# Kernel optimization log

Measured on AMD Instinct MI355X. Metric: run time of the kernel, lower is better.

## Reference

```python
import jax, jax.numpy as jnp
import numpy as np

D_MODEL = 512
H = 8


def setup_inputs() -> dict:
    key = jax.random.key(0)
    ks = jax.random.split(key, 11)
    B, L, D = 8, 1024, D_MODEL
    s = 1.0 / np.sqrt(D)
    return {
        "q": jax.random.normal(ks[0], (B, L, D), jnp.float32),
        "k": jax.random.normal(ks[1], (B, L, D), jnp.float32),
        "v": jax.random.normal(ks[2], (B, L, D), jnp.float32),
        "Wq": jax.random.normal(ks[3], (D, D), jnp.float32) * s,
        "bq": jnp.zeros((D,), jnp.float32),
        "Wk": jax.random.normal(ks[4], (D, D), jnp.float32) * s,
        "bk": jnp.zeros((D,), jnp.float32),
        "Wv": jax.random.normal(ks[5], (D, D), jnp.float32) * s,
        "bv": jnp.zeros((D,), jnp.float32),
        "Wo": jax.random.normal(ks[6], (D, D), jnp.float32) * s,
        "bo": jnp.zeros((D,), jnp.float32),
    }


def _split_heads(x, h):
    B, L, D = x.shape
    return x.reshape(B, L, h, D // h).transpose(0, 2, 1, 3)  # (B,h,L,dk)


def reference(q, k, v, Wq, bq, Wk, bk, Wv, bv, Wo, bo):
    B, L, D = q.shape
    dk = D // H
    qw = q @ Wq + bq
    kw = k @ Wk + bk
    vw = q @ Wv + bv  # faithful to source bug: dense_v applied to q, not v
    qh = _split_heads(qw, H)
    kh = _split_heads(kw, H)
    vh = _split_heads(vw, H)
    scale = jnp.asarray(1.0 / np.sqrt(dk), qh.dtype)
    scores = jnp.einsum("bhqd,bhkd->bhqk", qh, kh) * scale  # (B,h,L,L)
    attn = jax.nn.softmax(scores, axis=-1)
    ctx = jnp.einsum("bhqk,bhkd->bhqd", attn, vh)  # (B,h,L,dk)
    out = ctx.transpose(0, 2, 1, 3).reshape(B, L, D) @ Wo + bo
    return out, attn
```

## Files before the change

kernel.cpp:

```cpp
#include <hip/hip_runtime.h>

typedef unsigned short u16;
typedef __bf16 bf16x8 __attribute__((ext_vector_type(8)));
typedef unsigned short u16x8 __attribute__((ext_vector_type(8)));
typedef unsigned short u16x4 __attribute__((ext_vector_type(4)));
typedef float f32x4 __attribute__((ext_vector_type(4)));

#define MFMA16(a, b, c) __builtin_amdgcn_mfma_f32_16x16x32_bf16(a, b, c, 0, 0, 0)

__device__ __forceinline__ u16 f2bf(float f) {
    union { float f; unsigned u; } v; v.f = f;
    unsigned r = v.u + 0x7fffu + ((v.u >> 16) & 1u);
    return (u16)(r >> 16);
}
__device__ __forceinline__ float bf2f(u16 u) {
    union { unsigned u; float f; } v; v.u = (unsigned)u << 16;
    return v.f;
}

typedef __attribute__((address_space(1))) void GAS;
typedef __attribute__((address_space(3))) void LAS;
__device__ __forceinline__ void gload_lds16(const void* g, void* l) {
    __builtin_amdgcn_global_load_lds((GAS*)g, (LAS*)l, 16, 0, 0);
}

__global__ __launch_bounds__(256) void wtrans(const float* Wq, const float* Wk,
                                              const float* Wv, const float* Wo, u16* WT) {
    __shared__ float t[32][33];
    const int z = blockIdx.z;
    const float* W = (z == 0) ? Wq : (z == 1) ? Wk : (z == 2) ? Wv : Wo;
    u16* out = WT + (size_t)z * 512 * 512;
    const int tx = threadIdx.x, ty = threadIdx.y;
    const int k0 = blockIdx.y * 32, n0 = blockIdx.x * 32;
#pragma unroll
    for (int p = 0; p < 4; ++p)
        t[ty + 8 * p][tx] = W[(size_t)(k0 + ty + 8 * p) * 512 + n0 + tx];
    __syncthreads();
#pragma unroll
    for (int p = 0; p < 4; ++p) {
        const int n = n0 + ty + 8 * p;
        out[(size_t)n * 512 + k0 + tx] = f2bf(t[tx][ty + 8 * p]);
    }
}

__global__ __launch_bounds__(256) void qkconv(const float* q, const float* k, u16* qb, u16* kb) {
    const size_t n4 = (size_t)8192 * 512 / 4;
    const size_t stride = (size_t)gridDim.x * 256;
    for (size_t i = (size_t)blockIdx.x * 256 + threadIdx.x; i < 2 * n4; i += stride) {
        const float4 v = (i < n4) ? ((const float4*)q)[i] : ((const float4*)k)[i - n4];
        u16x4 o;
        o[0] = f2bf(v.x); o[1] = f2bf(v.y); o[2] = f2bf(v.z); o[3] = f2bf(v.w);
        if (i < n4) ((u16x4*)qb)[i] = o; else ((u16x4*)kb)[i - n4] = o;
    }
}

__global__ __launch_bounds__(256) void vtrans(const u16* vw, u16* vt) {
    __shared__ u16 t[64][72];
    const int l0 = blockIdx.x * 64, h = blockIdx.y, b = blockIdx.z;
    const int tid = threadIdx.x;
    {
        const int r = tid >> 2, c16 = (tid & 3) * 16;
        const u16* src = vw + (size_t)(b * 1024 + l0 + r) * 512 + h * 64 + c16;
        *(u16x8*)(&t[r][c16])     = *(const u16x8*)(src);
        *(u16x8*)(&t[r][c16 + 8]) = *(const u16x8*)(src + 8);
    }
    __syncthreads();
    {
        const int dk = tid >> 2, lc = (tid & 3) * 16;
        u16x8 a0, a1;
#pragma unroll
        for (int e = 0; e < 8; ++e) { a0[e] = t[lc + e][dk]; a1[e] = t[lc + 8 + e][dk]; }
        u16* dst = vt + ((size_t)(b * 8 + h) * 64 + dk) * 1024 + l0 + lc;
        *(u16x8*)dst       = a0;
        *(u16x8*)(dst + 8) = a1;
    }
}

template <bool C_F32>
__device__ __forceinline__ void gemm_core(const u16* A, const u16* Bt,
                                          const float* bias, void* Cp,
                                          int bm, int bn) {
    __shared__ u16 As[128 * 64];
    __shared__ u16 Bs[128 * 64];
    const int tid  = threadIdx.x;
    const int lane = tid & 63;
    const int w    = tid >> 6;
    const int wm   = (w >> 1) * 64;
    const int wn   = (w & 1) * 64;
    const int col  = lane & 15;
    const int quad = lane >> 4;
    const int srow = lane >> 3;
    const int scol = (lane & 7) * 8;

    f32x4 acc[4][4] = {};

    for (int kt = 0; kt < 512; kt += 64) {
        __syncthreads();
#pragma unroll
        for (int p = 0; p < 4; ++p) {
            const int c  = w * 4 + p;
            const int gr = c * 8 + srow;
            gload_lds16(A  + (size_t)(bm * 128 + gr) * 512 + kt + scol, As + c * 512);
            gload_lds16(Bt + (size_t)(bn * 128 + gr) * 512 + kt + scol, Bs + c * 512);
        }
        __syncthreads();
#pragma unroll
        for (int ks = 0; ks < 2; ++ks) {
            const int k0 = ks * 32 + quad * 8;
            bf16x8 af[4], bfr[4];
#pragma unroll
            for (int i = 0; i < 4; ++i)
                af[i] = __builtin_bit_cast(bf16x8, *(const u16x8*)(As + (wm + i * 16 + col) * 64 + k0));
#pragma unroll
            for (int j = 0; j < 4; ++j)
                bfr[j] = __builtin_bit_cast(bf16x8, *(const u16x8*)(Bs + (wn + j * 16 + col) * 64 + k0));
#pragma unroll
            for (int i = 0; i < 4; ++i)
#pragma unroll
                for (int j = 0; j < 4; ++j)
                    acc[i][j] = MFMA16(af[i], bfr[j], acc[i][j]);
        }
    }
#pragma unroll
    for (int j = 0; j < 4; ++j) {
        const int gn = bn * 128 + wn + j * 16 + col;
        const float bv = bias[gn];
#pragma unroll
        for (int i = 0; i < 4; ++i) {
#pragma unroll
            for (int r = 0; r < 4; ++r) {
                const int gm = bm * 128 + wm + i * 16 + quad * 4 + r;
                const float val = acc[i][j][r] + bv;
                if (C_F32) ((float*)Cp)[(size_t)gm * 512 + gn] = val;
                else       ((u16*)Cp)[(size_t)gm * 512 + gn]   = f2bf(val);
            }
        }
    }
}

__global__ __launch_bounds__(256, 3) void qkv_gemm(const u16* qb, const u16* kb, const u16* WT,
                                                   const float* bq, const float* bk, const float* bv,
                                                   u16* out) {
    const int z = blockIdx.z;
    const u16* A      = (z == 1) ? kb : qb;
    const u16* B      = WT + (size_t)z * 512 * 512;
    const float* bias = (z == 0) ? bq : (z == 1) ? bk : bv;
    u16* C            = out + (size_t)z * 8192 * 512;
    gemm_core<false>(A, B, bias, C, blockIdx.x, blockIdx.y);
}

__global__ __launch_bounds__(256, 3) void out_gemm(const u16* ctx, const u16* WoT,
                                                   const float* bo, float* out) {
    gemm_core<true>(ctx, WoT, bo, out, blockIdx.x, blockIdx.y);
}

__global__ __launch_bounds__(512, 4) void attn_kernel(const u16* qw, const u16* kw, const u16* vt,
                                                      float* attn_out, u16* ctx) {
    __shared__ u16 Ks[128 * 72];
    __shared__ u16 Vs[64 * 136];
    __shared__ u16 Ps[8][16 * 136];

    const int qt  = blockIdx.x;
    const int bh  = blockIdx.y;
    const int b   = bh >> 3, h = bh & 7;
    const int tid = threadIdx.x;
    const int lane = tid & 63, w = tid >> 6;
    const int col = lane & 15, quad = lane >> 4;
    const int wq  = w * 16;
    const float scale = 0.125f;

    const size_t headbase = (size_t)b * (1024 * 512) + (size_t)h * 64;
    const u16* vh = vt + (size_t)bh * (64 * 1024);

    const int krow = tid >> 2, koff = (tid & 3) * 16;
    const int vrow = tid >> 3, voff = (tid & 7) * 16;
    const u16* kbase = kw + headbase + (size_t)krow * 512 + koff;
    const u16* vbase = vh + (size_t)vrow * 1024 + voff;

    bf16x8 qf[2];
    {
        const u16* qp = qw + headbase + (size_t)(qt * 128 + wq + col) * 512 + quad * 8;
        qf[0] = __builtin_bit_cast(bf16x8, *(const u16x8*)qp);
        qf[1] = __builtin_bit_cast(bf16x8, *(const u16x8*)(qp + 32));
    }

    float l_acc[4] = {0.f, 0.f, 0.f, 0.f};

    u16x8 rk0 = *(const u16x8*)kbase;
    u16x8 rk1 = *(const u16x8*)(kbase + 8);
    for (int kt = 0; kt < 8; ++kt) {
        __syncthreads();
        *(u16x8*)(Ks + krow * 72 + koff)     = rk0;
        *(u16x8*)(Ks + krow * 72 + koff + 8) = rk1;
        __syncthreads();
        if (kt < 7) {
            const u16* kp = kbase + (size_t)(kt + 1) * (128 * 512);
            rk0 = *(const u16x8*)kp;
            rk1 = *(const u16x8*)(kp + 8);
        }
        f32x4 s[8] = {};
#pragma unroll
        for (int ks = 0; ks < 2; ++ks) {
            const int k0 = ks * 32 + quad * 8;
#pragma unroll
            for (int j = 0; j < 8; ++j) {
                const bf16x8 kf = __builtin_bit_cast(bf16x8,
                    *(const u16x8*)(Ks + (j * 16 + col) * 72 + k0));
                s[j] = MFMA16(qf[ks], kf, s[j]);
            }
        }
#pragma unroll
        for (int j = 0; j < 8; ++j)
#pragma unroll
            for (int r = 0; r < 4; ++r)
                l_acc[r] += __expf(s[j][r] * scale);
    }

    float rinv[4];
#pragma unroll
    for (int r = 0; r < 4; ++r) {
        float l = l_acc[r];
        l += __shfl_xor(l, 1); l += __shfl_xor(l, 2);
        l += __shfl_xor(l, 4); l += __shfl_xor(l, 8);
        rinv[r] = 1.0f / l;
    }

    f32x4 o[4] = {};

    rk0 = *(const u16x8*)kbase;
    rk1 = *(const u16x8*)(kbase + 8);
    u16x8 rv0 = *(const u16x8*)vbase;
    u16x8 rv1 = *(const u16x8*)(vbase + 8);
    for (int kt = 0; kt < 8; ++kt) {
        __syncthreads();
        *(u16x8*)(Ks + krow * 72 + koff)      = rk0;
        *(u16x8*)(Ks + krow * 72 + koff + 8)  = rk1;
        *(u16x8*)(Vs + vrow * 136 + voff)     = rv0;
        *(u16x8*)(Vs + vrow * 136 + voff + 8) = rv1;
        __syncthreads();
        if (kt < 7) {
            const u16* kp = kbase + (size_t)(kt + 1) * (128 * 512);
            rk0 = *(const u16x8*)kp;
            rk1 = *(const u16x8*)(kp + 8);
            const u16* vp = vbase + (kt + 1) * 128;
            rv0 = *(const u16x8*)vp;
            rv1 = *(const u16x8*)(vp + 8);
        }
        u16* pw = &Ps[w][0];
#pragma unroll
        for (int half = 0; half < 2; ++half) {
            f32x4 s[4] = {};
#pragma unroll
            for (int ks = 0; ks < 2; ++ks) {
                const int k0 = ks * 32 + quad * 8;
#pragma unroll
                for (int j = 0; j < 4; ++j) {
                    const bf16x8 kf = __builtin_bit_cast(bf16x8,
                        *(const u16x8*)(Ks + (half * 64 + j * 16 + col) * 72 + k0));
                    s[j] = MFMA16(qf[ks], kf, s[j]);
                }
            }
#pragma unroll
            for (int j = 0; j < 4; ++j)
#pragma unroll
                for (int r = 0; r < 4; ++r) {
                    const float p = __expf(s[j][r] * scale) * rinv[r];
                    pw[(quad * 4 + r) * 136 + half * 64 + j * 16 + col] = f2bf(p);
                }
        }
        {
            const int rl = lane >> 2, c0 = (lane & 3) * 4;
            float* ao = attn_out + ((size_t)bh * 1024 + (size_t)(qt * 128 + wq + rl)) * 1024
                        + (size_t)kt * 128 + c0;
#pragma unroll
            for (int it = 0; it < 8; ++it) {
                const u16x4 pv = *(const u16x4*)(pw + rl * 136 + it * 16 + c0);
                float4 f;
                f.x = bf2f(pv[0]); f.y = bf2f(pv[1]); f.z = bf2f(pv[2]); f.w = bf2f(pv[3]);
                *(float4*)(ao + it * 16) = f;
            }
        }
#pragma unroll
        for (int ks = 0; ks < 4; ++ks) {
            const int k0 = ks * 32 + quad * 8;
            const bf16x8 pf = __builtin_bit_cast(bf16x8, *(const u16x8*)(pw + col * 136 + k0));
#pragma unroll
            for (int j = 0; j < 4; ++j) {
                const bf16x8 vf = __builtin_bit_cast(bf16x8,
                    *(const u16x8*)(Vs + (j * 16 + col) * 136 + k0));
                o[j] = MFMA16(pf, vf, o[j]);
            }
        }
    }

#pragma unroll
    for (int j = 0; j < 4; ++j)
#pragma unroll
        for (int r = 0; r < 4; ++r) {
            const int qg = qt * 128 + wq + quad * 4 + r;
            ctx[(size_t)(b * 1024 + qg) * 512 + h * 64 + j * 16 + col] = f2bf(o[j][r]);
        }
}

extern "C" void kernel_launch(void* const* d_in, const int* in_sizes, int n_in,
                              void* d_out, int out_size, void* d_ws, size_t ws_size,
                              hipStream_t stream) {
    (void)in_sizes; (void)n_in; (void)out_size; (void)ws_size;
    const float* q  = (const float*)d_in[0];
    const float* k  = (const float*)d_in[1];
    const float* Wq = (const float*)d_in[3];
    const float* bq = (const float*)d_in[4];
    const float* Wk = (const float*)d_in[5];
    const float* bk = (const float*)d_in[6];
    const float* Wv = (const float*)d_in[7];
    const float* bv = (const float*)d_in[8];
    const float* Wo = (const float*)d_in[9];
    const float* bo = (const float*)d_in[10];

    float* out  = (float*)d_out;
    float* attn = (float*)d_out + (size_t)8 * 1024 * 512;

    char* ws = (char*)d_ws;
    u16* WT  = (u16*)ws;
    u16* qb  = (u16*)(ws + (size_t)2 * 1024 * 1024);
    u16* kb  = qb + (size_t)8192 * 512;
    u16* qkv = kb + (size_t)8192 * 512;
    u16* qw  = qkv;
    u16* kw  = qkv + (size_t)8192 * 512;
    u16* vw  = qkv + (size_t)2 * 8192 * 512;
    u16* ctx = qkv + (size_t)3 * 8192 * 512;
    u16* vt  = qkv + (size_t)4 * 8192 * 512;

    wtrans     <<<dim3(16, 16, 4), dim3(32, 8), 0, stream>>>(Wq, Wk, Wv, Wo, WT);
    qkconv     <<<dim3(2048),      256,          0, stream>>>(q, k, qb, kb);
    qkv_gemm   <<<dim3(64, 4, 3),  256,          0, stream>>>(qb, kb, WT, bq, bk, bv, qkv);
    vtrans     <<<dim3(16, 8, 8),  256,          0, stream>>>(vw, vt);
    attn_kernel<<<dim3(8, 64),     512,          0, stream>>>(qw, kw, vt, attn, ctx);
    out_gemm   <<<dim3(64, 4),     256,          0, stream>>>(ctx, WT + (size_t)3 * 512 * 512, bo, out);
}
```

Baseline: 415.7 us.

## Transpose score MFMA layout, vectorize P stores, nontemporal attn writes, swap grid order

Swaps the MFMA operands so each lane holds four consecutive key columns of one query row. The row-sum reduction then needs fewer shuffles, and P can be written to LDS as packed 4-element vectors instead of scattered scalar stores. The attention-matrix write-out now has each half-wave cover a full 128-column row segment, which gives contiguous 512-byte stores, and uses nontemporal stores to avoid polluting the cache. The launch grid is reordered so consecutive blocks span different heads, and bf16 rounding moves to the hardware conversion builtin.

```diff
diff --git a/kernel.cpp b/kernel.cpp
--- a/kernel.cpp
+++ b/kernel.cpp
@@ -16,6 +16,9 @@
 __device__ __forceinline__ float bf2f(u16 u) {
     union { unsigned u; float f; } v; v.u = (unsigned)u << 16;
     return v.f;
+}
+__device__ __forceinline__ u16 bfc(float f) {
+    return __builtin_bit_cast(u16, (__bf16)f);
 }
 
 typedef __attribute__((address_space(1))) void GAS;
@@ -160,8 +163,8 @@
     __shared__ u16 Vs[64 * 136];
     __shared__ u16 Ps[8][16 * 136];
 
-    const int qt  = blockIdx.x;
-    const int bh  = blockIdx.y;
+    const int bh  = blockIdx.x;
+    const int qt  = blockIdx.y;
     const int b   = bh >> 3, h = bh & 7;
     const int tid = threadIdx.x;
     const int lane = tid & 63, w = tid >> 6;
@@ -184,7 +187,7 @@
         qf[1] = __builtin_bit_cast(bf16x8, *(const u16x8*)(qp + 32));
     }
 
-    float l_acc[4] = {0.f, 0.f, 0.f, 0.f};
+    float l_acc = 0.f;
 
     u16x8 rk0 = *(const u16x8*)kbase;
     u16x8 rk1 = *(const u16x8*)(kbase + 8);
@@ -206,23 +209,21 @@
             for (int j = 0; j < 8; ++j) {
                 const bf16x8 kf = __builtin_bit_cast(bf16x8,
                     *(const u16x8*)(Ks + (j * 16 + col) * 72 + k0));
-                s[j] = MFMA16(qf[ks], kf, s[j]);
+                s[j] = MFMA16(kf, qf[ks], s[j]);
             }
         }
 #pragma unroll
         for (int j = 0; j < 8; ++j)
 #pragma unroll
             for (int r = 0; r < 4; ++r)
-                l_acc[r] += __expf(s[j][r] * scale);
-    }
-
-    float rinv[4];
-#pragma unroll
-    for (int r = 0; r < 4; ++r) {
-        float l = l_acc[r];
-        l += __shfl_xor(l, 1); l += __shfl_xor(l, 2);
-        l += __shfl_xor(l, 4); l += __shfl_xor(l, 8);
-        rinv[r] = 1.0f / l;
+                l_acc += __expf(s[j][r] * scale);
+    }
+
+    float rinv;
+    {
+        float l = l_acc;
+        l += __shfl_xor(l, 16); l += __shfl_xor(l, 32);
+        rinv = 1.0f / l;
     }
 
     f32x4 o[4] = {};
@@ -257,27 +258,31 @@
                 for (int j = 0; j < 4; ++j) {
                     const bf16x8 kf = __builtin_bit_cast(bf16x8,
                         *(const u16x8*)(Ks + (half * 64 + j * 16 + col) * 72 + k0));
-                    s[j] = MFMA16(qf[ks], kf, s[j]);
+                    s[j] = MFMA16(kf, qf[ks], s[j]);
                 }
             }
 #pragma unroll
-            for (int j = 0; j < 4; ++j)
-#pragma unroll
-                for (int r = 0; r < 4; ++r) {
-                    const float p = __expf(s[j][r] * scale) * rinv[r];
-                    pw[(quad * 4 + r) * 136 + half * 64 + j * 16 + col] = f2bf(p);
-                }
+            for (int j = 0; j < 4; ++j) {
+                u16x4 pk;
+                pk[0] = bfc(__expf(s[j][0] * scale) * rinv);
+                pk[1] = bfc(__expf(s[j][1] * scale) * rinv);
+                pk[2] = bfc(__expf(s[j][2] * scale) * rinv);
+                pk[3] = bfc(__expf(s[j][3] * scale) * rinv);
+                *(u16x4*)(pw + col * 136 + half * 64 + j * 16 + quad * 4) = pk;
+            }
         }
         {
-            const int rl = lane >> 2, c0 = (lane & 3) * 4;
-            float* ao = attn_out + ((size_t)bh * 1024 + (size_t)(qt * 128 + wq + rl)) * 1024
-                        + (size_t)kt * 128 + c0;
+            const int r2 = lane >> 5;
+            const int c0 = (lane & 31) * 4;
+            float* ao = attn_out + ((size_t)bh * 1024 + (size_t)(qt * 128 + wq)) * 1024
+                        + (size_t)kt * 128;
 #pragma unroll
             for (int it = 0; it < 8; ++it) {
-                const u16x4 pv = *(const u16x4*)(pw + rl * 136 + it * 16 + c0);
-                float4 f;
-                f.x = bf2f(pv[0]); f.y = bf2f(pv[1]); f.z = bf2f(pv[2]); f.w = bf2f(pv[3]);
-                *(float4*)(ao + it * 16) = f;
+                const int row = it * 2 + r2;
+                const u16x4 pv = *(const u16x4*)(pw + row * 136 + c0);
+                f32x4 f;
+                f[0] = bf2f(pv[0]); f[1] = bf2f(pv[1]); f[2] = bf2f(pv[2]); f[3] = bf2f(pv[3]);
+                __builtin_nontemporal_store(f, (f32x4*)(ao + (size_t)row * 1024 + c0));
             }
         }
 #pragma unroll
@@ -335,6 +340,6 @@
     qkconv     <<<dim3(2048),      256,          0, stream>>>(q, k, qb, kb);
     qkv_gemm   <<<dim3(64, 4, 3),  256,          0, stream>>>(qb, kb, WT, bq, bk, bv, qkv);
     vtrans     <<<dim3(16, 8, 8),  256,          0, stream>>>(vw, vt);
-    attn_kernel<<<dim3(8, 64),     512,          0, stream>>>(qw, kw, vt, attn, ctx);
+    attn_kernel<<<dim3(64, 8),     512,          0, stream>>>(qw, kw, vt, attn, ctx);
     out_gemm   <<<dim3(64, 4),     256,          0, stream>>>(ctx, WT + (size_t)3 * 512 * 512, bo, out);
 }
```

New measurement: 410.6 us. No clear change (-1.2%).
